# Performance work log

Hardware: AMD Instinct MI355X
Metric: run time of the kernel (lower is better)

The kernel has to match this reference:

```python
import jax, jax.numpy as jnp
import numpy as np

K = 3            # kernel size
C_IN = 8
C_OUT = 16
PATCH = C_IN * K * K  # 72
EPS = 1e-6


def setup_inputs() -> dict:
    key = jax.random.key(0)
    k1, k2, k3 = jax.random.split(key, 3)
    in_tensor = jax.random.normal(k1, (4, C_IN, 112, 112), dtype=jnp.float32)
    # 1x1-conv weighting predictor: C_in -> PATCH*C_OUT channels
    w_pred = jax.random.normal(k2, (PATCH * C_OUT, C_IN), dtype=jnp.float32) * 0.05
    b_pred = jax.random.normal(k3, (PATCH * C_OUT,), dtype=jnp.float32) * 0.05
    return {"in_tensor": in_tensor, "w_pred": w_pred, "b_pred": b_pred}


def reference(in_tensor, w_pred, b_pred):
    B, C, H, W = in_tensor.shape
    # --- weighting module: predict dynamic weights per spatial location ---
    raw = jnp.einsum('bchw,oc->bohw', in_tensor, w_pred) + b_pred[None, :, None, None]
    weightings = raw.reshape(B, PATCH, C_OUT, H, W)          # [B, C*k*k, C_out, H, W]
    # norm = L2 norm of the dynamic weight over the patch dim -> [B, C_out, H, W]
    norm = jnp.sqrt(jnp.sum(weightings * weightings, axis=1)) + EPS
    # --- unfold: overlapping k x k patches, same padding, stride 1 ---
    patches = jax.lax.conv_general_dilated_patches(
        in_tensor, (K, K), (1, 1), 'SAME')                   # [B, C*k*k, H, W]
    # --- weighted sum over the patch dim, then normalize ---
    activations = jnp.einsum('bphw,bpohw->bohw', patches, weightings)  # [B, C_out, H, W]
    return activations / norm
```

## Files before the change

### kernel.cpp

```cpp
#include <hip/hip_runtime.h>
#include <math.h>

#define IMG_W 112
#define HW    12544
#define CI    8
#define CO    16
#define NP    72
#define EPS   1e-6f

typedef __attribute__((ext_vector_type(8))) short short8;
typedef __attribute__((ext_vector_type(4))) float f32x4;

static __device__ inline short f2bf(float f) {
  unsigned u = __float_as_uint(f);
  return (short)((u + 0x7FFFu + ((u >> 16) & 1u)) >> 16);
}

static constexpr int DQ[9] = {-113, -112, -111, -1, 0, 1, 111, 112, 113};

__global__ __launch_bounds__(512) void coda_mfma(
    const float* __restrict__ in, const float* __restrict__ wp,
    const float* __restrict__ bp, float* __restrict__ out)
{
  __shared__ short sA[NP][32][8];
  __shared__ float sBuf[CI * 290];
  __shared__ short sZ[16];

  const int tid = threadIdx.x;
  const int b   = blockIdx.x / 196;
  const int r0  = (blockIdx.x - b * 196) * 64;
  const float* __restrict__ inb = in + b * CI * HW;

  for (int idx = tid; idx < NP * 32; idx += 512) {
    const int p = idx >> 5, l = idx & 31, q = l >> 4, m = l & 15;
    const int row = p * 16 + m;
    short8 v = {0, 0, 0, 0, 0, 0, 0, 0};
    if (q == 0) {
      const float* wr = wp + row * CI;
#pragma unroll
      for (int j = 0; j < 8; ++j) v[j] = f2bf(wr[j]);
    } else {
      v[0] = f2bf(bp[row]);
    }
    *(short8*)&sA[p][l][0] = v;
  }
  if (tid < 16) sZ[tid] = 0;
  for (int k = tid; k < CI * 290; k += 512) {
    const int c = k / 290;
    const int i = k - c * 290;
    int gg = r0 - 113 + i;
    gg = (gg < 0) ? 0 : (gg > HW - 1 ? HW - 1 : gg);
    sBuf[k] = inb[c * HW + gg];
  }
  __syncthreads();

  const int wave = tid >> 6;
  const int lane = tid & 63;
  const int g    = wave & 3;
  const int half = wave >> 2;
  const int ln   = lane & 15;
  const int quad = lane >> 4;
  const int rwav = r0 + g * 16;
  const int h    = rwav / IMG_W;
  const int wl   = (rwav - h * IMG_W) + ln;
  const int off  = g * 16 + ln + 113;

  float vm[9];
#pragma unroll
  for (int q = 0; q < 9; ++q) {
    const int kh = q / 3, kw = q % 3;
    const bool ok = ((unsigned)(h + kh - 1) < 112u) &&
                    ((unsigned)(wl + kw - 1) < 112u);
    vm[q] = ok ? 1.f : 0.f;
  }

  short8 bf = {0, 0, 0, 0, 0, 0, 0, 0};
#pragma unroll
  for (int j = 0; j < 8; ++j) {
    const short bv = f2bf(sBuf[j * 290 + off]);
    bf[j] = (quad == 0) ? bv : ((quad == 1 && j == 0) ? (short)0x3F80 : (short)0);
  }

  float acc[4] = {0.f, 0.f, 0.f, 0.f};
  float n2[4]  = {0.f, 0.f, 0.f, 0.f};
  const bool qlo = (quad < 2);
  const int  c0  = half * 4;

#pragma unroll
  for (int cc = 0; cc < 4; ++cc) {
    const int c = c0 + cc;
    const float* __restrict__ sc = &sBuf[c * 290 + off];
#pragma unroll
    for (int q = 0; q < 9; ++q) {
      const int p = c * 9 + q;
      const short* ap = qlo ? &sA[p][quad * 16 + ln][0] : &sZ[0];
      const short8 af = *(const short8*)ap;
      const float pv = vm[q] * sc[DQ[q]];
      const f32x4 zc = {0.f, 0.f, 0.f, 0.f};
      const f32x4 d = __builtin_amdgcn_mfma_f32_16x16x32_bf16(af, bf, zc, 0, 0, 0);
#pragma unroll
      for (int i = 0; i < 4; ++i) {
        acc[i] = fmaf(pv, d[i], acc[i]);
        n2[i]  = fmaf(d[i], d[i], n2[i]);
      }
    }
  }

  __syncthreads();
  if (half == 1) {
#pragma unroll
    for (int i = 0; i < 4; ++i) {
      sBuf[i * 256 + g * 64 + lane]       = acc[i];
      sBuf[(i + 4) * 256 + g * 64 + lane] = n2[i];
    }
  }
  __syncthreads();
  if (half == 0) {
    float* __restrict__ ob = out + (long)b * CO * HW + rwav + ln;
#pragma unroll
    for (int i = 0; i < 4; ++i) {
      const float a2 = acc[i] + sBuf[i * 256 + g * 64 + lane];
      const float s2 = n2[i] + sBuf[(i + 4) * 256 + g * 64 + lane];
      const int co = quad * 4 + i;
      ob[(long)co * HW] = a2 / (sqrtf(s2) + EPS);
    }
  }
}

extern "C" void kernel_launch(void* const* d_in, const int* in_sizes, int n_in,
                              void* d_out, int out_size, void* d_ws, size_t ws_size,
                              hipStream_t stream) {
  const float* in = (const float*)d_in[0];
  const float* wp = (const float*)d_in[1];
  const float* bp = (const float*)d_in[2];
  float* out = (float*)d_out;

  coda_mfma<<<dim3(784), dim3(512), 0, stream>>>(in, wp, bp, out);
}
```

Before: 72.11 us.

## Switch to fp16 16x16x16 MFMA and batch independent MFMAs per channel

Replaces the bf16 16x16x32 MFMA, which was mostly zero-padded in K, with the fp16 16x16x16 variant. The K dimension is now packed as 8 weights plus a bias row across three quads. The kernel hoists all patch values into registers up front, issues nine independent MFMAs per channel before consuming their results so the MFMA latency can overlap, and adds a min-blocks launch bound. The aim is to shorten MFMA latency and dependency stalls. In exchange it uses more registers and lowers precision from bf16 to fp16 range.

```diff
diff --git a/kernel.cpp b/kernel.cpp
--- a/kernel.cpp
+++ b/kernel.cpp
@@ -8,43 +8,42 @@
 #define NP    72
 #define EPS   1e-6f
 
-typedef __attribute__((ext_vector_type(8))) short short8;
+typedef __attribute__((ext_vector_type(4))) _Float16 half4;
 typedef __attribute__((ext_vector_type(4))) float f32x4;
-
-static __device__ inline short f2bf(float f) {
-  unsigned u = __float_as_uint(f);
-  return (short)((u + 0x7FFFu + ((u >> 16) & 1u)) >> 16);
-}
 
 static constexpr int DQ[9] = {-113, -112, -111, -1, 0, 1, 111, 112, 113};
 
-__global__ __launch_bounds__(512) void coda_mfma(
+__global__ __launch_bounds__(512, 4) void coda_mfma(
     const float* __restrict__ in, const float* __restrict__ wp,
     const float* __restrict__ bp, float* __restrict__ out)
 {
-  __shared__ short sA[NP][32][8];
+  __shared__ half4 sA[NP][48];
   __shared__ float sBuf[CI * 290];
-  __shared__ short sZ[16];
+  __shared__ half4 sZ[1];
 
   const int tid = threadIdx.x;
   const int b   = blockIdx.x / 196;
   const int r0  = (blockIdx.x - b * 196) * 64;
   const float* __restrict__ inb = in + b * CI * HW;
 
-  for (int idx = tid; idx < NP * 32; idx += 512) {
-    const int p = idx >> 5, l = idx & 31, q = l >> 4, m = l & 15;
+  for (int idx = tid; idx < NP * 48; idx += 512) {
+    const int p = idx / 48, l = idx - p * 48;
+    const int quad = l >> 4, m = l & 15;
     const int row = p * 16 + m;
-    short8 v = {0, 0, 0, 0, 0, 0, 0, 0};
-    if (q == 0) {
-      const float* wr = wp + row * CI;
+    half4 v = {(_Float16)0, (_Float16)0, (_Float16)0, (_Float16)0};
+    if (quad < 2) {
+      const float* wr = wp + row * CI + quad * 4;
 #pragma unroll
-      for (int j = 0; j < 8; ++j) v[j] = f2bf(wr[j]);
+      for (int j = 0; j < 4; ++j) v[j] = (_Float16)wr[j];
     } else {
-      v[0] = f2bf(bp[row]);
+      v[0] = (_Float16)bp[row];
     }
-    *(short8*)&sA[p][l][0] = v;
+    sA[p][l] = v;
   }
-  if (tid < 16) sZ[tid] = 0;
+  if (tid == 0) {
+    half4 z = {(_Float16)0, (_Float16)0, (_Float16)0, (_Float16)0};
+    sZ[0] = z;
+  }
   for (int k = tid; k < CI * 290; k += 512) {
     const int c = k / 290;
     const int i = k - c * 290;
@@ -74,34 +73,49 @@
     vm[q] = ok ? 1.f : 0.f;
   }
 
-  short8 bf = {0, 0, 0, 0, 0, 0, 0, 0};
+  const int c0 = half * 4;
+
+  float pv[4][9];
 #pragma unroll
-  for (int j = 0; j < 8; ++j) {
-    const short bv = f2bf(sBuf[j * 290 + off]);
-    bf[j] = (quad == 0) ? bv : ((quad == 1 && j == 0) ? (short)0x3F80 : (short)0);
+  for (int cc = 0; cc < 4; ++cc)
+#pragma unroll
+    for (int q = 0; q < 9; ++q)
+      pv[cc][q] = vm[q] * sBuf[(c0 + cc) * 290 + off + DQ[q]];
+
+  half4 bf = {(_Float16)0, (_Float16)0, (_Float16)0, (_Float16)0};
+  if (quad < 2) {
+#pragma unroll
+    for (int j = 0; j < 4; ++j)
+      bf[j] = (_Float16)sBuf[(quad * 4 + j) * 290 + off];
+  } else if (quad == 2) {
+    bf[0] = (_Float16)1.0f;
   }
 
   float acc[4] = {0.f, 0.f, 0.f, 0.f};
   float n2[4]  = {0.f, 0.f, 0.f, 0.f};
-  const bool qlo = (quad < 2);
-  const int  c0  = half * 4;
+
+  const half4* __restrict__ abase = (quad < 3) ? &sA[0][quad * 16 + ln] : &sZ[0];
+  const int astep = (quad < 3) ? 48 : 0;
 
 #pragma unroll
   for (int cc = 0; cc < 4; ++cc) {
     const int c = c0 + cc;
-    const float* __restrict__ sc = &sBuf[c * 290 + off];
+    half4 af[9];
+#pragma unroll
+    for (int q = 0; q < 9; ++q) af[q] = abase[(c * 9 + q) * astep];
+    f32x4 d[9];
 #pragma unroll
     for (int q = 0; q < 9; ++q) {
-      const int p = c * 9 + q;
-      const short* ap = qlo ? &sA[p][quad * 16 + ln][0] : &sZ[0];
-      const short8 af = *(const short8*)ap;
-      const float pv = vm[q] * sc[DQ[q]];
       const f32x4 zc = {0.f, 0.f, 0.f, 0.f};
-      const f32x4 d = __builtin_amdgcn_mfma_f32_16x16x32_bf16(af, bf, zc, 0, 0, 0);
+      d[q] = __builtin_amdgcn_mfma_f32_16x16x16f16(af[q], bf, zc, 0, 0, 0);
+    }
+#pragma unroll
+    for (int q = 0; q < 9; ++q) {
+      const float p_ = pv[cc][q];
 #pragma unroll
       for (int i = 0; i < 4; ++i) {
-        acc[i] = fmaf(pv, d[i], acc[i]);
-        n2[i]  = fmaf(d[i], d[i], n2[i]);
+        acc[i] = fmaf(p_, d[q][i], acc[i]);
+        n2[i]  = fmaf(d[q][i], d[q][i], n2[i]);
       }
     }
   }
```

After: 73.28 us. About the same (+1.6%).
